# Kernel optimization log

Hardware: AMD Instinct MI355X
Metric: run time of the kernel (lower is better)

Reference implementation:

```python
import jax, jax.numpy as jnp
import numpy as np

T, B, D_IN, D_H, D_OUT = 16, 8192, 512, 1024, 256


def setup_inputs() -> dict:
    key = jax.random.key(0)
    ks = jax.random.split(key, 4)
    # He-style scaled init to keep activations sane
    x = jax.random.normal(ks[0], (B, D_IN), dtype=jnp.float32)
    W1 = jax.random.normal(ks[1], (T, D_IN, D_H), dtype=jnp.float32) / np.sqrt(D_IN)
    b1 = jnp.zeros((T, D_H), dtype=jnp.float32)
    W2 = jax.random.normal(ks[2], (T, D_H, D_H), dtype=jnp.float32) / np.sqrt(D_H)
    b2 = jnp.zeros((T, D_H), dtype=jnp.float32)
    W3 = jax.random.normal(ks[3], (T, D_H, D_OUT), dtype=jnp.float32) / np.sqrt(D_H)
    b3 = jnp.zeros((T, D_OUT), dtype=jnp.float32)
    return {"x": x, "W1": W1, "b1": b1, "W2": W2, "b2": b2, "W3": W3, "b3": b3}


def reference(x, W1, b1, W2, b2, W3, b3):
    # Batched over the tree dimension t: one grouped GEMM per layer instead of
    # a Python loop over trees.
    h = jax.nn.relu(jnp.einsum('bi,tih->tbh', x, W1) + b1[:, None, :])   # [T,B,H]
    h = jax.nn.relu(jnp.einsum('tbh,thk->tbk', h, W2) + b2[:, None, :])  # [T,B,H]
    out = jnp.einsum('tbh,tho->tbo', h, W3) + b3[:, None, :]             # [T,B,O]
    return jnp.mean(out, axis=0)                                          # [B,O]
```

## Files before the change

### kernel.cpp

```cpp
#include <hip/hip_runtime.h>
#include <hip/hip_bf16.h>
#include <stdint.h>

#define T_TREES 16
#define B_ROWS  8192
#define DIN     512
#define DH      1024
#define DOUT    256

typedef unsigned short u16;
typedef __attribute__((ext_vector_type(8))) short short8;
typedef __attribute__((ext_vector_type(16))) float floatx16;

__device__ __forceinline__ u16 f2bf(float f) {
    union { float f; uint32_t u; } v; v.f = f;
    uint32_t u = v.u;
    uint32_t r = (u + 0x7fffu + ((u >> 16) & 1u)) >> 16;
    return (u16)r;
}

__device__ __forceinline__ void async_copy16(const u16* g, u16* l) {
    __builtin_amdgcn_global_load_lds(
        (const __attribute__((address_space(1))) uint32_t*)g,
        (__attribute__((address_space(3))) uint32_t*)l,
        16, 0, 0);
}

__global__ void prep_kernel(const float* __restrict__ x, u16* __restrict__ xb,
                            const float* __restrict__ b3, float* __restrict__ out,
                            const float* __restrict__ W1, const float* __restrict__ W2,
                            const float* __restrict__ W3,
                            u16* __restrict__ W1b, u16* __restrict__ W2b,
                            u16* __restrict__ W3b) {
    __shared__ float tile[32][33];
    if (blockIdx.x < 4096) {
        int idx = blockIdx.x * 256 + threadIdx.x;
        float4 v = ((const float4*)x)[idx];
        ushort4 o;
        o.x = f2bf(v.x); o.y = f2bf(v.y); o.z = f2bf(v.z); o.w = f2bf(v.w);
        ((ushort4*)xb)[idx] = o;
    } else if (blockIdx.x < 12288) {
        int idx = (blockIdx.x - 4096) * 256 + threadIdx.x;
        int o = idx & (DOUT - 1);
        float s = 0.f;
#pragma unroll
        for (int t = 0; t < T_TREES; t++) s += b3[t * DOUT + o];
        out[idx] = s * (1.f / T_TREES);
    } else {
        int bid = blockIdx.x - 12288;
        int t = bid / 1792, tl = bid - t * 1792;
        const float* in; u16* outp; int K, N, kt, nt; float scale = 1.f;
        if (tl < 512)       { in = W1; outp = W1b; K = DIN; N = DH;   kt = tl & 15; nt = tl >> 4; }
        else if (tl < 1536) { tl -= 512;  in = W2; outp = W2b; K = DH; N = DH;   kt = tl & 31; nt = tl >> 5; }
        else                { tl -= 1536; in = W3; outp = W3b; K = DH; N = DOUT; kt = tl & 31; nt = tl >> 5;
                              scale = 1.f / T_TREES; }
        int k0 = kt * 32, n0 = nt * 32;
        const float* inb = in + (size_t)t * K * N;
        u16* outb = outp + (size_t)t * K * N;
        int c = threadIdx.x & 31, rg = threadIdx.x >> 5;
#pragma unroll
        for (int i = 0; i < 4; i++) {
            int r = rg * 4 + i;
            tile[r][c] = inb[(size_t)(k0 + r) * N + n0 + c];
        }
        __syncthreads();
#pragma unroll
        for (int i = 0; i < 4; i++) {
            int r = rg * 4 + i;
            outb[(size_t)(n0 + r) * K + k0 + c] = f2bf(tile[c][r] * scale);
        }
    }
}

__global__ void reduce_kernel(const float* __restrict__ Part, float* __restrict__ Out, int g) {
    int idx = blockIdx.x * 256 + threadIdx.x;
    float4 s = ((const float4*)Out)[idx];
    for (int t = 0; t < g; t++) {
        float4 p = ((const float4*)(Part + (size_t)t * B_ROWS * DOUT))[idx];
        s.x += p.x; s.y += p.y; s.z += p.z; s.w += p.w;
    }
    ((float4*)Out)[idx] = s;
}


#define GEMM_PREAMBLE_COMMON()                               \
    const int tid  = threadIdx.x;                            \
    const int wave = tid >> 6;                               \
    const int lane = tid & 63;                               \
    const int l31  = lane & 31;                              \
    const int h    = lane >> 5;                              \
    const int rg   = tid >> 3;                               \
    const int colE = (((tid & 7) ^ (rg & 7)) << 3);          \
    const int xm   = l31 & 7;

#define STAGE256(kt_, p_)                                                              \
    {                                                                                  \
        const int k0_ = (kt_) * 64;                                                    \
        u16* lA_ = lds + (p_) * 32768 + wave * 512;                                    \
        u16* lB_ = lA_ + 16384;                                                        \
        _Pragma("unroll")                                                              \
        for (int j_ = 0; j_ < 4; j_++) {                                               \
            const int row_ = j_ * 64 + rg;                                             \
            async_copy16(Ab + (size_t)(m0 + row_) * K + k0_ + colE, lA_ + j_ * 4096);  \
            async_copy16(Bb + (size_t)(n0 + row_) * K + k0_ + colE, lB_ + j_ * 4096);  \
        }                                                                              \
    }

#define COMPUTE256(p_)                                                                 \
    {                                                                                  \
        const u16* A_ = lds + (p_) * 32768;                                            \
        const u16* B_ = A_ + 16384;                                                    \
        short8 bfr[2][4];                                                              \
        _Pragma("unroll")                                                              \
        for (int nf = 0; nf < 2; nf++) {                                               \
            const int r_ = wn4 * 64 + nf * 32 + l31;                                   \
            _Pragma("unroll")                                                          \
            for (int kk = 0; kk < 4; kk++)                                             \
                bfr[nf][kk] = *(const short8*)&B_[r_ * 64 + (((kk * 2 + h) ^ xm) << 3)]; \
        }                                                                              \
        _Pragma("unroll")                                                              \
        for (int mh = 0; mh < 2; mh++) {                                               \
            short8 afr[2][4];                                                          \
            _Pragma("unroll")                                                          \
            for (int mf = 0; mf < 2; mf++) {                                           \
                const int r_ = wm2 * 128 + mh * 64 + mf * 32 + l31;                    \
                _Pragma("unroll")                                                      \
                for (int kk = 0; kk < 4; kk++)                                         \
                    afr[mf][kk] = *(const short8*)&A_[r_ * 64 + (((kk * 2 + h) ^ xm) << 3)]; \
            }                                                                          \
            __builtin_amdgcn_s_setprio(1);                                             \
            _Pragma("unroll")                                                          \
            for (int kk = 0; kk < 4; kk++)                                             \
                _Pragma("unroll")                                                      \
                for (int mf = 0; mf < 2; mf++)                                         \
                    _Pragma("unroll")                                                  \
                    for (int nf = 0; nf < 2; nf++)                                     \
                        acc[mh * 2 + mf][nf] = __builtin_amdgcn_mfma_f32_32x32x16_bf16(\
                            afr[mf][kk], bfr[nf][kk], acc[mh * 2 + mf][nf], 0, 0, 0);  \
            __builtin_amdgcn_s_setprio(0);                                             \
        }                                                                              \
    }

#define GEMM_MAIN(STAGE_, COMPUTE_)                                              \
    STAGE_(0, 0);                                                                \
    STAGE_(1, 1);                                                                \
    for (int kt = 0; kt < NT; kt++) {                                            \
        const int p_ = kt & 1;                                                   \
        if (kt < NT - 1) asm volatile("s_waitcnt vmcnt(8)\n\ts_barrier" ::: "memory"); \
        else             asm volatile("s_waitcnt vmcnt(0)\n\ts_barrier" ::: "memory"); \
        COMPUTE_(p_);                                                            \
        asm volatile("s_barrier" ::: "memory");                                  \
        if (kt + 2 < NT) STAGE_(kt + 2, p_);                                     \
    }

__global__ __launch_bounds__(512, 2)
void gemm_l2_256(const u16* __restrict__ A, size_t aStrideT,
                 const u16* __restrict__ Bt,
                 const float* __restrict__ bias,
                 u16* __restrict__ C,
                 int M, int N, int K) {
    extern __shared__ u16 lds[];

    const int t = blockIdx.z;
    const u16* Ab = A + (size_t)t * aStrideT;
    const u16* Bb = Bt + (size_t)t * (size_t)N * K;
    u16* Cb = C + (size_t)t * (size_t)M * N;
    const float* biasb = bias + (size_t)t * N;

    const int m0 = blockIdx.x * 256;
    const int n0 = blockIdx.y * 256;

    GEMM_PREAMBLE_COMMON();
    const int wm2 = wave >> 2;
    const int wn4 = wave & 3;

    floatx16 acc[4][2];
#pragma unroll
    for (int ai = 0; ai < 4; ai++)
#pragma unroll
        for (int nf = 0; nf < 2; nf++)
#pragma unroll
            for (int r = 0; r < 16; r++) acc[ai][nf][r] = 0.f;

    const int NT = K >> 6;
    GEMM_MAIN(STAGE256, COMPUTE256);

#pragma unroll
    for (int nf = 0; nf < 2; nf++) {
        const int n = n0 + wn4 * 64 + nf * 32 + l31;
        const float bv = biasb[n];
#pragma unroll
        for (int ai = 0; ai < 4; ai++) {
#pragma unroll
            for (int r = 0; r < 16; r++) {
                const int m = m0 + wm2 * 128 + ai * 32 + (r & 3) + 8 * (r >> 2) + 4 * h;
                float v = acc[ai][nf][r] + bv;
                v = v > 0.f ? v : 0.f;
                Cb[(size_t)m * N + n] = f2bf(v);
            }
        }
    }
}

#define STAGE128(kt_, p_)                                                              \
    {                                                                                  \
        const int k0_ = (kt_) * 64;                                                    \
        u16* lA_ = lds + (p_) * 16384 + wave * 512;                                    \
        u16* lB_ = lA_ + 8192;                                                         \
        _Pragma("unroll")                                                              \
        for (int j_ = 0; j_ < 4; j_++) {                                               \
            const int row_ = j_ * 32 + rg;                                             \
            async_copy16(Ab + (size_t)(m0 + row_) * K + k0_ + colE, lA_ + j_ * 2048);  \
            async_copy16(Bb + (size_t)(n0 + row_) * K + k0_ + colE, lB_ + j_ * 2048);  \
        }                                                                              \
    }

#define COMPUTE128(p_)                                                                 \
    {                                                                                  \
        const u16* A_ = lds + (p_) * 16384;                                            \
        const u16* B_ = A_ + 8192;                                                     \
        short8 bfr[2][4], afr[2][4];                                                   \
        _Pragma("unroll")                                                              \
        for (int nf = 0; nf < 2; nf++) {                                               \
            const int r_ = wn + nf * 32 + l31;                                         \
            _Pragma("unroll")                                                          \
            for (int kk = 0; kk < 4; kk++)                                             \
                bfr[nf][kk] = *(const short8*)&B_[r_ * 64 + (((kk * 2 + h) ^ xm) << 3)]; \
        }                                                                              \
        _Pragma("unroll")                                                              \
        for (int mf = 0; mf < 2; mf++) {                                               \
            const int r_ = wm + mf * 32 + l31;                                         \
            _Pragma("unroll")                                                          \
            for (int kk = 0; kk < 4; kk++)                                             \
                afr[mf][kk] = *(const short8*)&A_[r_ * 64 + (((kk * 2 + h) ^ xm) << 3)]; \
        }                                                                              \
        __builtin_amdgcn_s_setprio(1);                                                 \
        _Pragma("unroll")                                                              \
        for (int kk = 0; kk < 4; kk++)                                                 \
            _Pragma("unroll")                                                          \
            for (int mf = 0; mf < 2; mf++)                                             \
                _Pragma("unroll")                                                      \
                for (int nf = 0; nf < 2; nf++)                                         \
                    acc[mf][nf] = __builtin_amdgcn_mfma_f32_32x32x16_bf16(             \
                        afr[mf][kk], bfr[nf][kk], acc[mf][nf], 0, 0, 0);               \
        __builtin_amdgcn_s_setprio(0);                                                 \
    }

__global__ __launch_bounds__(256, 2)
void gemm_l1_128(const u16* __restrict__ A, size_t aStrideT,
                 const u16* __restrict__ Bt,
                 const float* __restrict__ bias,
                 u16* __restrict__ C,
                 int M, int N, int K) {
    extern __shared__ u16 lds[];

    const int t = blockIdx.z;
    const u16* Ab = A + (size_t)t * aStrideT;
    const u16* Bb = Bt + (size_t)t * (size_t)N * K;
    u16* Cb = C + (size_t)t * (size_t)M * N;
    const float* biasb = bias + (size_t)t * N;

    const int m0 = blockIdx.x * 128;
    const int n0 = blockIdx.y * 128;

    GEMM_PREAMBLE_COMMON();
    const int wm = (wave >> 1) * 64;
    const int wn = (wave & 1) * 64;

    floatx16 acc[2][2];
#pragma unroll
    for (int mf = 0; mf < 2; mf++)
#pragma unroll
        for (int nf = 0; nf < 2; nf++)
#pragma unroll
            for (int r = 0; r < 16; r++) acc[mf][nf][r] = 0.f;

    const int NT = K >> 6;
    GEMM_MAIN(STAGE128, COMPUTE128);

#pragma unroll
    for (int nf = 0; nf < 2; nf++) {
        const int n = n0 + wn + nf * 32 + l31;
        const float bv = biasb[n];
#pragma unroll
        for (int mf = 0; mf < 2; mf++) {
#pragma unroll
            for (int r = 0; r < 16; r++) {
                const int m = m0 + wm + mf * 32 + (r & 3) + 8 * (r >> 2) + 4 * h;
                float v = acc[mf][nf][r] + bv;
                v = v > 0.f ? v : 0.f;
                Cb[(size_t)m * N + n] = f2bf(v);
            }
        }
    }
}

__global__ __launch_bounds__(256, 2)
void gemm_l3_128(const u16* __restrict__ H2, const u16* __restrict__ W3t,
                 float* __restrict__ Part) {
    constexpr int M = B_ROWS, N = DOUT, K = DH;
    extern __shared__ u16 lds[];

    const int m0 = blockIdx.x * 128;
    const int n0 = blockIdx.y * 128;
    const int t = blockIdx.z;
    const u16* Ab = H2 + (size_t)t * M * K;
    const u16* Bb = W3t + (size_t)t * N * K;
    float* Pb = Part + (size_t)t * M * N;

    GEMM_PREAMBLE_COMMON();
    const int wm = (wave >> 1) * 64;
    const int wn = (wave & 1) * 64;

    floatx16 acc[2][2];
#pragma unroll
    for (int mf = 0; mf < 2; mf++)
#pragma unroll
        for (int nf = 0; nf < 2; nf++)
#pragma unroll
            for (int r = 0; r < 16; r++) acc[mf][nf][r] = 0.f;

    const int NT = K >> 6;
    GEMM_MAIN(STAGE128, COMPUTE128);

#pragma unroll
    for (int nf = 0; nf < 2; nf++) {
        const int n = n0 + wn + nf * 32 + l31;
#pragma unroll
        for (int mf = 0; mf < 2; mf++) {
#pragma unroll
            for (int r = 0; r < 16; r++) {
                const int m = m0 + wm + mf * 32 + (r & 3) + 8 * (r >> 2) + 4 * h;
                Pb[(size_t)m * N + n] = acc[mf][nf][r];
            }
        }
    }
}

extern "C" void kernel_launch(void* const* d_in, const int* in_sizes, int n_in,
                              void* d_out, int out_size, void* d_ws, size_t ws_size,
                              hipStream_t stream) {
    const float* x  = (const float*)d_in[0];
    const float* W1 = (const float*)d_in[1];
    const float* b1 = (const float*)d_in[2];
    const float* W2 = (const float*)d_in[3];
    const float* b2 = (const float*)d_in[4];
    const float* W3 = (const float*)d_in[5];
    const float* b3 = (const float*)d_in[6];
    float* out = (float*)d_out;

    const size_t XB_BYTES = 8388608ull;
    const size_t W1B_BYTES = 16777216ull, W2B_BYTES = 33554432ull, W3B_BYTES = 8388608ull;
    const size_t FIXED = XB_BYTES + W1B_BYTES + W2B_BYTES + W3B_BYTES;
    const size_t PER_TREE = 33554432ull;

    uint8_t* ws = (uint8_t*)d_ws;
    u16* xb  = (u16*)ws;
    u16* W1b = (u16*)(ws + XB_BYTES);
    u16* W2b = (u16*)(ws + XB_BYTES + W1B_BYTES);
    u16* W3b = (u16*)(ws + XB_BYTES + W1B_BYTES + W2B_BYTES);
    u16* h1  = (u16*)(ws + FIXED);
    float* part = (float*)(ws + FIXED);

    int g = 16;
    while (g > 1 && FIXED + (size_t)g * PER_TREE > ws_size) g >>= 1;
    const int nG = T_TREES / g;
    u16* h2 = (u16*)(ws + FIXED + (size_t)g * (PER_TREE / 2));

    prep_kernel<<<12288 + 1792 * T_TREES, 256, 0, stream>>>(
        x, xb, b3, out, W1, W2, W3, W1b, W2b, W3b);

    const uint32_t LDS256 = 131072;
    const uint32_t LDS128 = 65536;

    for (int gi = 0; gi < nG; gi++) {
        const int t0 = gi * g;
        gemm_l1_128<<<dim3(B_ROWS / 128, DH / 128, g), 256, LDS128, stream>>>(
            xb, 0, W1b + (size_t)t0 * DIN * DH, b1 + (size_t)t0 * DH, h1, B_ROWS, DH, DIN);
        gemm_l2_256<<<dim3(B_ROWS / 256, DH / 256, g), 512, LDS256, stream>>>(
            h1, (size_t)B_ROWS * DH, W2b + (size_t)t0 * DH * DH, b2 + (size_t)t0 * DH, h2, B_ROWS, DH, DH);
        gemm_l3_128<<<dim3(B_ROWS / 128, DOUT / 128, g), 256, LDS128, stream>>>(
            h2, W3b + (size_t)t0 * DH * DOUT, part);
        reduce_kernel<<<(B_ROWS * DOUT / 4) / 256, 256, 0, stream>>>(part, out, g);
    }
}
```

Baseline: 831.5 us.

## Accumulate two trees per block in layer-3 GEMM and vectorize weight-transpose loads

The layer-3 GEMM now runs its K loop across two trees' hidden activations and weights in one block, accumulating their contributions in registers. This halves the partial-sum buffer the kernel writes and the reduce kernel reads. The price is half as many blocks in the grid, each running a K loop twice as long. The prep kernel's weight-transpose load also switches to float4 global reads in place of scalar loads.

```diff
diff --git a/kernel.cpp b/kernel.cpp
--- a/kernel.cpp
+++ b/kernel.cpp
@@ -57,13 +57,14 @@
         int k0 = kt * 32, n0 = nt * 32;
         const float* inb = in + (size_t)t * K * N;
         u16* outb = outp + (size_t)t * K * N;
+        int c4 = threadIdx.x & 7, rr = threadIdx.x >> 3;
+        float4 v = *(const float4*)&inb[(size_t)(k0 + rr) * N + n0 + c4 * 4];
+        tile[rr][c4 * 4 + 0] = v.x;
+        tile[rr][c4 * 4 + 1] = v.y;
+        tile[rr][c4 * 4 + 2] = v.z;
+        tile[rr][c4 * 4 + 3] = v.w;
+        __syncthreads();
         int c = threadIdx.x & 31, rg = threadIdx.x >> 5;
-#pragma unroll
-        for (int i = 0; i < 4; i++) {
-            int r = rg * 4 + i;
-            tile[r][c] = inb[(size_t)(k0 + r) * N + n0 + c];
-        }
-        __syncthreads();
 #pragma unroll
         for (int i = 0; i < 4; i++) {
             int r = rg * 4 + i;
@@ -215,6 +216,22 @@
         }                                                                              \
     }
 
+#define STAGE_L3(kt_, p_)                                                              \
+    {                                                                                  \
+        const int lt_ = ltBase + ((kt_) >> 4);                                         \
+        const int k0_ = ((kt_) & 15) * 64;                                             \
+        const u16* At_ = H2g + (size_t)lt_ * B_ROWS * DH;                              \
+        const u16* Bt_ = W3g + (size_t)lt_ * DOUT * DH;                                \
+        u16* lA_ = lds + (p_) * 16384 + wave * 512;                                    \
+        u16* lB_ = lA_ + 8192;                                                         \
+        _Pragma("unroll")                                                              \
+        for (int j_ = 0; j_ < 4; j_++) {                                               \
+            const int row_ = j_ * 32 + rg;                                             \
+            async_copy16(At_ + (size_t)(m0 + row_) * DH + k0_ + colE, lA_ + j_ * 2048);\
+            async_copy16(Bt_ + (size_t)(n0 + row_) * DH + k0_ + colE, lB_ + j_ * 2048);\
+        }                                                                              \
+    }
+
 #define COMPUTE128(p_)                                                                 \
     {                                                                                  \
         const u16* A_ = lds + (p_) * 16384;                                            \
@@ -296,17 +313,14 @@
 }
 
 __global__ __launch_bounds__(256, 2)
-void gemm_l3_128(const u16* __restrict__ H2, const u16* __restrict__ W3t,
-                 float* __restrict__ Part) {
-    constexpr int M = B_ROWS, N = DOUT, K = DH;
+void gemm_l3_ts(const u16* __restrict__ H2g, const u16* __restrict__ W3g,
+                float* __restrict__ Part, int treesPerBlock) {
     extern __shared__ u16 lds[];
 
     const int m0 = blockIdx.x * 128;
     const int n0 = blockIdx.y * 128;
-    const int t = blockIdx.z;
-    const u16* Ab = H2 + (size_t)t * M * K;
-    const u16* Bb = W3t + (size_t)t * N * K;
-    float* Pb = Part + (size_t)t * M * N;
+    const int ltBase = blockIdx.z * treesPerBlock;
+    float* Pb = Part + (size_t)blockIdx.z * B_ROWS * DOUT;
 
     GEMM_PREAMBLE_COMMON();
     const int wm = (wave >> 1) * 64;
@@ -320,8 +334,8 @@
 #pragma unroll
             for (int r = 0; r < 16; r++) acc[mf][nf][r] = 0.f;
 
-    const int NT = K >> 6;
-    GEMM_MAIN(STAGE128, COMPUTE128);
+    const int NT = treesPerBlock << 4;
+    GEMM_MAIN(STAGE_L3, COMPUTE128);
 
 #pragma unroll
     for (int nf = 0; nf < 2; nf++) {
@@ -331,7 +345,7 @@
 #pragma unroll
             for (int r = 0; r < 16; r++) {
                 const int m = m0 + wm + mf * 32 + (r & 3) + 8 * (r >> 2) + 4 * h;
-                Pb[(size_t)m * N + n] = acc[mf][nf][r];
+                Pb[(size_t)m * DOUT + n] = acc[mf][nf][r];
             }
         }
     }
@@ -373,14 +387,17 @@
     const uint32_t LDS256 = 131072;
     const uint32_t LDS128 = 65536;
 
+    const int tpb = (g >= 2) ? 2 : 1;
+    const int zd = g / tpb;
+
     for (int gi = 0; gi < nG; gi++) {
         const int t0 = gi * g;
         gemm_l1_128<<<dim3(B_ROWS / 128, DH / 128, g), 256, LDS128, stream>>>(
             xb, 0, W1b + (size_t)t0 * DIN * DH, b1 + (size_t)t0 * DH, h1, B_ROWS, DH, DIN);
         gemm_l2_256<<<dim3(B_ROWS / 256, DH / 256, g), 512, LDS256, stream>>>(
             h1, (size_t)B_ROWS * DH, W2b + (size_t)t0 * DH * DH, b2 + (size_t)t0 * DH, h2, B_ROWS, DH, DH);
-        gemm_l3_128<<<dim3(B_ROWS / 128, DOUT / 128, g), 256, LDS128, stream>>>(
-            h2, W3b + (size_t)t0 * DH * DOUT, part);
-        reduce_kernel<<<(B_ROWS * DOUT / 4) / 256, 256, 0, stream>>>(part, out, g);
-    }
-}
+        gemm_l3_ts<<<dim3(B_ROWS / 128, DOUT / 128, zd), 256, LDS128, stream>>>(
+            h2, W3b + (size_t)t0 * DH * DOUT, part, tpb);
+        reduce_kernel<<<(B_ROWS * DOUT / 4) / 256, 256, 0, stream>>>(part, out, zd);
+    }
+}
```

Measured after the change: 804.9 us. 1.03x faster.

## Use 256x256 tiles for layer-3 GEMM and vectorize weight transpose

Applied to the files above, without the earlier changes.

Layer 3 now runs on the 256x256, 512-thread GEMM kernel already used for layer 2, with one block covering all 256 output columns. Each H2 row tile is then loaded once instead of twice, which halves reads of the large activation tensor. The weight-prep transpose now loads float4 and writes 16-byte packed bf16 stores. In exchange, layer 3 launches fewer blocks per tree and each uses more LDS.

```diff
diff --git a/kernel.cpp b/kernel.cpp
--- a/kernel.cpp
+++ b/kernel.cpp
@@ -57,17 +57,21 @@
         int k0 = kt * 32, n0 = nt * 32;
         const float* inb = in + (size_t)t * K * N;
         u16* outb = outp + (size_t)t * K * N;
-        int c = threadIdx.x & 31, rg = threadIdx.x >> 5;
-#pragma unroll
-        for (int i = 0; i < 4; i++) {
-            int r = rg * 4 + i;
-            tile[r][c] = inb[(size_t)(k0 + r) * N + n0 + c];
-        }
+        int c4 = threadIdx.x & 7, rr = threadIdx.x >> 3;
+        float4 v = *(const float4*)&inb[(size_t)(k0 + rr) * N + n0 + c4 * 4];
+        tile[rr][c4 * 4 + 0] = v.x;
+        tile[rr][c4 * 4 + 1] = v.y;
+        tile[rr][c4 * 4 + 2] = v.z;
+        tile[rr][c4 * 4 + 3] = v.w;
         __syncthreads();
-#pragma unroll
-        for (int i = 0; i < 4; i++) {
-            int r = rg * 4 + i;
-            outb[(size_t)(n0 + r) * K + k0 + c] = f2bf(tile[c][r] * scale);
+        if (threadIdx.x < 128) {
+            int n  = threadIdx.x >> 2;
+            int kq = threadIdx.x & 3;
+            short8 o;
+#pragma unroll
+            for (int j = 0; j < 8; j++)
+                ((u16*)&o)[j] = f2bf(tile[kq * 8 + j][n] * scale);
+            *(short8*)&outb[(size_t)(n0 + n) * K + k0 + kq * 8] = o;
         }
     }
 }
@@ -202,6 +206,49 @@
     }
 }
 
+__global__ __launch_bounds__(512, 2)
+void gemm_l3_256(const u16* __restrict__ H2, const u16* __restrict__ W3t,
+                 float* __restrict__ Part) {
+    constexpr int M = B_ROWS, N = DOUT, K = DH;
+    extern __shared__ u16 lds[];
+
+    const int t = blockIdx.z;
+    const u16* Ab = H2 + (size_t)t * M * K;
+    const u16* Bb = W3t + (size_t)t * (size_t)N * K;
+    float* Pb = Part + (size_t)t * (size_t)M * N;
+
+    const int m0 = blockIdx.x * 256;
+    const int n0 = 0;
+
+    GEMM_PREAMBLE_COMMON();
+    const int wm2 = wave >> 2;
+    const int wn4 = wave & 3;
+
+    floatx16 acc[4][2];
+#pragma unroll
+    for (int ai = 0; ai < 4; ai++)
+#pragma unroll
+        for (int nf = 0; nf < 2; nf++)
+#pragma unroll
+            for (int r = 0; r < 16; r++) acc[ai][nf][r] = 0.f;
+
+    const int NT = K >> 6;
+    GEMM_MAIN(STAGE256, COMPUTE256);
+
+#pragma unroll
+    for (int nf = 0; nf < 2; nf++) {
+        const int n = n0 + wn4 * 64 + nf * 32 + l31;
+#pragma unroll
+        for (int ai = 0; ai < 4; ai++) {
+#pragma unroll
+            for (int r = 0; r < 16; r++) {
+                const int m = m0 + wm2 * 128 + ai * 32 + (r & 3) + 8 * (r >> 2) + 4 * h;
+                Pb[(size_t)m * N + n] = acc[ai][nf][r];
+            }
+        }
+    }
+}
+
 #define STAGE128(kt_, p_)                                                              \
     {                                                                                  \
         const int k0_ = (kt_) * 64;                                                    \
@@ -290,48 +337,6 @@
                 float v = acc[mf][nf][r] + bv;
                 v = v > 0.f ? v : 0.f;
                 Cb[(size_t)m * N + n] = f2bf(v);
-            }
-        }
-    }
-}
-
-__global__ __launch_bounds__(256, 2)
-void gemm_l3_128(const u16* __restrict__ H2, const u16* __restrict__ W3t,
-                 float* __restrict__ Part) {
-    constexpr int M = B_ROWS, N = DOUT, K = DH;
-    extern __shared__ u16 lds[];
-
-    const int m0 = blockIdx.x * 128;
-    const int n0 = blockIdx.y * 128;
-    const int t = blockIdx.z;
-    const u16* Ab = H2 + (size_t)t * M * K;
-    const u16* Bb = W3t + (size_t)t * N * K;
-    float* Pb = Part + (size_t)t * M * N;
-
-    GEMM_PREAMBLE_COMMON();
-    const int wm = (wave >> 1) * 64;
-    const int wn = (wave & 1) * 64;
-
-    floatx16 acc[2][2];
-#pragma unroll
-    for (int mf = 0; mf < 2; mf++)
-#pragma unroll
-        for (int nf = 0; nf < 2; nf++)
-#pragma unroll
-            for (int r = 0; r < 16; r++) acc[mf][nf][r] = 0.f;
-
-    const int NT = K >> 6;
-    GEMM_MAIN(STAGE128, COMPUTE128);
-
-#pragma unroll
-    for (int nf = 0; nf < 2; nf++) {
-        const int n = n0 + wn + nf * 32 + l31;
-#pragma unroll
-        for (int mf = 0; mf < 2; mf++) {
-#pragma unroll
-            for (int r = 0; r < 16; r++) {
-                const int m = m0 + wm + mf * 32 + (r & 3) + 8 * (r >> 2) + 4 * h;
-                Pb[(size_t)m * N + n] = acc[mf][nf][r];
             }
         }
     }
@@ -379,7 +384,7 @@
             xb, 0, W1b + (size_t)t0 * DIN * DH, b1 + (size_t)t0 * DH, h1, B_ROWS, DH, DIN);
         gemm_l2_256<<<dim3(B_ROWS / 256, DH / 256, g), 512, LDS256, stream>>>(
             h1, (size_t)B_ROWS * DH, W2b + (size_t)t0 * DH * DH, b2 + (size_t)t0 * DH, h2, B_ROWS, DH, DH);
-        gemm_l3_128<<<dim3(B_ROWS / 128, DOUT / 128, g), 256, LDS128, stream>>>(
+        gemm_l3_256<<<dim3(B_ROWS / 256, 1, g), 512, LDS256, stream>>>(
             h2, W3b + (size_t)t0 * DH * DOUT, part);
         reduce_kernel<<<(B_ROWS * DOUT / 4) / 256, 256, 0, stream>>>(part, out, g);
     }
```

After: 845.2 us. No clear change (+1.7%).
